# Optimization experiments

Measured on AMD Instinct MI355X. Metric: run time of the kernel, lower is better.

Reference implementation:

```python
import jax, jax.numpy as jnp
import numpy as np

N_LOC, D_IN = 100000, 128
N_ROUTES, ROUTE_LEN = 8192, 100
D_OUT = 256
LN_EPS = 1e-5


def setup_inputs() -> dict:
    key = jax.random.key(0)
    k1, k2, k3 = jax.random.split(key, 3)
    graph_embedding = jax.random.normal(k1, (N_LOC, D_IN), dtype=jnp.float32)
    locations_idx = jax.random.randint(k2, (N_ROUTES, ROUTE_LEN), 0, N_LOC, dtype=jnp.int64)
    W = jax.random.normal(k3, (D_IN, D_OUT), dtype=jnp.float32) / np.sqrt(D_IN)
    b = jnp.zeros((D_OUT,), dtype=jnp.float32)
    gamma = jnp.ones((D_OUT,), dtype=jnp.float32)
    beta = jnp.zeros((D_OUT,), dtype=jnp.float32)
    return {"graph_embedding": graph_embedding, "locations_idx": locations_idx,
            "W": W, "b": b, "gamma": gamma, "beta": beta}


def reference(graph_embedding, locations_idx, W, b, gamma, beta):
    # Gather per-route node embeddings: [n_routes, route_len, D_in]
    gathered = graph_embedding[locations_idx]
    # Max-pool over the route dimension -> [n_routes, D_in]
    pooled = jnp.max(gathered, axis=1)
    # LinearBlockWithNormalization: Linear -> LayerNorm -> ReLU
    h = pooled @ W + b  # [n_routes, D_out]
    mu = jnp.mean(h, axis=-1, keepdims=True)
    var = jnp.mean(jnp.square(h - mu), axis=-1, keepdims=True)
    hn = (h - mu) * jax.lax.rsqrt(var + LN_EPS) * gamma + beta
    return jax.nn.relu(hn)
```

## Files before the change

kernel.cpp:

```cpp
#include <hip/hip_runtime.h>
#include <math.h>

constexpr int N_LOC     = 100000;
constexpr int D_IN      = 128;
constexpr int N_ROUTES  = 8192;
constexpr int ROUTE_LEN = 100;
constexpr int D_OUT     = 256;
constexpr float LN_EPS  = 1e-5f;

constexpr int RPB      = 4;
constexpr int NTHREADS = 256;
constexpr size_t EMB_ELEMS = (size_t)N_LOC * D_IN;
constexpr size_t F16_BYTES = EMB_ELEMS * 2;

typedef __fp16 f16x2 __attribute__((ext_vector_type(2)));

__device__ inline unsigned pk_max_f16(unsigned a, unsigned b) {
    unsigned d;
    asm("v_pk_max_f16 %0, %1, %2" : "=v"(d) : "v"(a), "v"(b));
    return d;
}

__global__ __launch_bounds__(256, 8)
void convert_f16_kernel(const float* __restrict__ emb, unsigned* __restrict__ emb16) {
    size_t i = ((size_t)blockIdx.x * blockDim.x + threadIdx.x) * 4;
    const size_t stride = (size_t)gridDim.x * blockDim.x * 4;
    for (; i < EMB_ELEMS; i += stride) {
        const float4 v = *reinterpret_cast<const float4*>(emb + i);
        const f16x2 a = __builtin_amdgcn_cvt_pkrtz(v.x, v.y);
        const f16x2 b = __builtin_amdgcn_cvt_pkrtz(v.z, v.w);
        uint2 u;
        u.x = __builtin_bit_cast(unsigned, a);
        u.y = __builtin_bit_cast(unsigned, b);
        *reinterpret_cast<uint2*>(emb16 + i / 2) = u;
    }
}

template<bool F16>
__global__ __launch_bounds__(NTHREADS, 8)
void routes_encoder_kernel(const float*    __restrict__ emb,
                           const unsigned* __restrict__ emb16,
                           const int*      __restrict__ idx,
                           const float*    __restrict__ W,
                           const float*    __restrict__ bias,
                           const float*    __restrict__ gamma,
                           const float*    __restrict__ beta,
                           float*          __restrict__ out)
{
    __shared__ int   s_idx[RPB * ROUTE_LEN];
    __shared__ float s_pooled[RPB][D_IN];
    __shared__ float s_sum[4][RPB];
    __shared__ float s_ssq[4][RPB];

    const int tid    = threadIdx.x;
    const int route0 = blockIdx.x * RPB;

    for (int i = tid; i < RPB * ROUTE_LEN; i += NTHREADS)
        s_idx[i] = idx[(size_t)route0 * ROUTE_LEN + i];
    __syncthreads();

    const int w    = tid >> 6;
    const int lane = tid & 63;

    if constexpr (F16) {
        const int q  = lane >> 4;
        const int dc = (lane & 15) * 8;
        const int* gi = &s_idx[w * ROUTE_LEN];
        unsigned m0 = 0xFC00FC00u, m1 = m0, m2 = m0, m3 = m0;
        #pragma unroll 5
        for (int t = 0; t < ROUTE_LEN / 4; ++t) {
            const int row = gi[4 * t + q];
            const uint4 v = *reinterpret_cast<const uint4*>(
                emb16 + ((size_t)row * D_IN + dc) / 2);
            m0 = pk_max_f16(m0, v.x);
            m1 = pk_max_f16(m1, v.y);
            m2 = pk_max_f16(m2, v.z);
            m3 = pk_max_f16(m3, v.w);
        }
        #pragma unroll
        for (int off = 32; off >= 16; off >>= 1) {
            m0 = pk_max_f16(m0, (unsigned)__shfl_down((int)m0, off));
            m1 = pk_max_f16(m1, (unsigned)__shfl_down((int)m1, off));
            m2 = pk_max_f16(m2, (unsigned)__shfl_down((int)m2, off));
            m3 = pk_max_f16(m3, (unsigned)__shfl_down((int)m3, off));
        }
        if (lane < 16) {
            const f16x2 h0 = __builtin_bit_cast(f16x2, m0);
            const f16x2 h1 = __builtin_bit_cast(f16x2, m1);
            const f16x2 h2 = __builtin_bit_cast(f16x2, m2);
            const f16x2 h3 = __builtin_bit_cast(f16x2, m3);
            *reinterpret_cast<float4*>(&s_pooled[w][dc]) =
                make_float4((float)h0.x, (float)h0.y, (float)h1.x, (float)h1.y);
            *reinterpret_cast<float4*>(&s_pooled[w][dc + 4]) =
                make_float4((float)h2.x, (float)h2.y, (float)h3.x, (float)h3.y);
        }
    } else {
        const int* gi = &s_idx[w * ROUTE_LEN];
        float2 m = make_float2(-INFINITY, -INFINITY);
        #pragma unroll 10
        for (int l = 0; l < ROUTE_LEN; ++l) {
            const float2 v = *reinterpret_cast<const float2*>(
                emb + (size_t)gi[l] * D_IN + lane * 2);
            m.x = fmaxf(m.x, v.x);
            m.y = fmaxf(m.y, v.y);
        }
        *reinterpret_cast<float2*>(&s_pooled[w][lane * 2]) = m;
    }
    __syncthreads();

    float h[RPB];
    {
        const float bo = bias[tid];
        #pragma unroll
        for (int r = 0; r < RPB; ++r) h[r] = bo;

        #pragma unroll 8
        for (int k = 0; k < D_IN; k += 4) {
            const float wk0 = W[(size_t)(k + 0) * D_OUT + tid];
            const float wk1 = W[(size_t)(k + 1) * D_OUT + tid];
            const float wk2 = W[(size_t)(k + 2) * D_OUT + tid];
            const float wk3 = W[(size_t)(k + 3) * D_OUT + tid];
            #pragma unroll
            for (int r = 0; r < RPB; ++r) {
                const float4 p = *reinterpret_cast<const float4*>(&s_pooled[r][k]);
                h[r] = fmaf(p.x, wk0, h[r]);
                h[r] = fmaf(p.y, wk1, h[r]);
                h[r] = fmaf(p.z, wk2, h[r]);
                h[r] = fmaf(p.w, wk3, h[r]);
            }
        }
    }

    float s[RPB], ss[RPB];
    #pragma unroll
    for (int r = 0; r < RPB; ++r) { s[r] = h[r]; ss[r] = h[r] * h[r]; }

    #pragma unroll
    for (int off = 32; off > 0; off >>= 1) {
        #pragma unroll
        for (int r = 0; r < RPB; ++r) {
            s[r]  += __shfl_down(s[r],  off);
            ss[r] += __shfl_down(ss[r], off);
        }
    }
    if (lane == 0) {
        #pragma unroll
        for (int r = 0; r < RPB; ++r) { s_sum[w][r] = s[r]; s_ssq[w][r] = ss[r]; }
    }
    __syncthreads();

    const float gm = gamma[tid];
    const float bt = beta[tid];
    #pragma unroll
    for (int r = 0; r < RPB; ++r) {
        const float tot = s_sum[0][r] + s_sum[1][r] + s_sum[2][r] + s_sum[3][r];
        const float tsq = s_ssq[0][r] + s_ssq[1][r] + s_ssq[2][r] + s_ssq[3][r];
        const float mu  = tot * (1.0f / D_OUT);
        const float var = tsq * (1.0f / D_OUT) - mu * mu;
        const float inv = rsqrtf(var + LN_EPS);
        const float y   = fmaxf((h[r] - mu) * inv * gm + bt, 0.0f);
        __builtin_nontemporal_store(y, &out[(size_t)(route0 + r) * D_OUT + tid]);
    }
}

extern "C" void kernel_launch(void* const* d_in, const int* in_sizes, int n_in,
                              void* d_out, int out_size, void* d_ws, size_t ws_size,
                              hipStream_t stream) {
    const float* emb   = (const float*)d_in[0];
    const int*   idx   = (const int*)  d_in[1];
    const float* W     = (const float*)d_in[2];
    const float* bias  = (const float*)d_in[3];
    const float* gamma = (const float*)d_in[4];
    const float* beta  = (const float*)d_in[5];
    float* out = (float*)d_out;

    if (ws_size >= F16_BYTES) {
        unsigned* emb16 = (unsigned*)d_ws;
        convert_f16_kernel<<<dim3(2048), dim3(256), 0, stream>>>(emb, emb16);
        routes_encoder_kernel<true><<<dim3(N_ROUTES / RPB), dim3(NTHREADS), 0, stream>>>(
            emb, emb16, idx, W, bias, gamma, beta, out);
    } else {
        routes_encoder_kernel<false><<<dim3(N_ROUTES / RPB), dim3(NTHREADS), 0, stream>>>(
            emb, nullptr, idx, W, bias, gamma, beta, out);
    }
}
```

Before: 139.9 us.

## Split gather-max into row-range passes for cache locality, then reduce partials

The embedding table is split into 8 row ranges, and a new pass computes per-route partial maxima using only indices inside each range, selected via ballot masks. The idea is that each range's slice of the fp16 table stays resident in cache. A second pass combines the 8 partials and runs the linear, LayerNorm and ReLU epilogue. In exchange it launches 8x more blocks, scans indices redundantly, serializes the per-index loads within each wave, and writes and reads an extra partial buffer.

```diff
diff --git a/kernel.cpp b/kernel.cpp
--- a/kernel.cpp
+++ b/kernel.cpp
@@ -8,10 +8,14 @@
 constexpr int D_OUT     = 256;
 constexpr float LN_EPS  = 1e-5f;
 
+constexpr int NRANGE   = 8;
+constexpr int RSIZE    = N_LOC / NRANGE;
 constexpr int RPB      = 4;
 constexpr int NTHREADS = 256;
-constexpr size_t EMB_ELEMS = (size_t)N_LOC * D_IN;
-constexpr size_t F16_BYTES = EMB_ELEMS * 2;
+constexpr size_t EMB_ELEMS  = (size_t)N_LOC * D_IN;
+constexpr size_t F16_BYTES  = EMB_ELEMS * 2;
+constexpr size_t PART_U32S  = (size_t)NRANGE * N_ROUTES * (D_IN / 2);
+constexpr size_t PART_BYTES = PART_U32S * 4;
 
 typedef __fp16 f16x2 __attribute__((ext_vector_type(2)));
 
@@ -33,6 +37,134 @@
         u.x = __builtin_bit_cast(unsigned, a);
         u.y = __builtin_bit_cast(unsigned, b);
         *reinterpret_cast<uint2*>(emb16 + i / 2) = u;
+    }
+}
+
+__global__ __launch_bounds__(NTHREADS, 8)
+void pass_a_kernel(const unsigned* __restrict__ emb16,
+                   const int*      __restrict__ idx,
+                   unsigned*       __restrict__ part)
+{
+    __shared__ int s_idx[RPB * ROUTE_LEN];
+
+    const int tid    = threadIdx.x;
+    const int range  = blockIdx.x & (NRANGE - 1);
+    const int rgrp   = blockIdx.x >> 3;
+    const int route0 = rgrp * RPB;
+
+    for (int i = tid; i < RPB * ROUTE_LEN; i += NTHREADS)
+        s_idx[i] = idx[(size_t)route0 * ROUTE_LEN + i];
+    __syncthreads();
+
+    const int w    = tid >> 6;
+    const int lane = tid & 63;
+    const int* gi  = &s_idx[w * ROUTE_LEN];
+    const int  lo  = range * RSIZE;
+
+    const int i0 = gi[lane];
+    const int i1 = (lane < ROUTE_LEN - 64) ? gi[64 + lane] : -1;
+    unsigned long long m0 = __ballot((unsigned)(i0 - lo) < (unsigned)RSIZE);
+    unsigned long long m1 = __ballot(i1 >= 0 && (unsigned)(i1 - lo) < (unsigned)RSIZE);
+
+    unsigned acc0 = 0xFC00FC00u, acc1 = 0xFC00FC00u;
+    while (m0 | m1) {
+        if (m0) {
+            const int l = __ffsll((unsigned long long)m0) - 1; m0 &= m0 - 1;
+            const unsigned v = emb16[(size_t)gi[l] * (D_IN / 2) + lane];
+            acc0 = pk_max_f16(acc0, v);
+        }
+        if (m1) {
+            const int l = __ffsll((unsigned long long)m1) - 1; m1 &= m1 - 1;
+            const unsigned v = emb16[(size_t)gi[64 + l] * (D_IN / 2) + lane];
+            acc1 = pk_max_f16(acc1, v);
+        }
+    }
+    const unsigned acc = pk_max_f16(acc0, acc1);
+    __builtin_nontemporal_store(
+        acc, &part[((size_t)range * N_ROUTES + route0 + w) * (D_IN / 2) + lane]);
+}
+
+__global__ __launch_bounds__(NTHREADS, 8)
+void pass_b_kernel(const unsigned* __restrict__ part,
+                   const float*    __restrict__ W,
+                   const float*    __restrict__ bias,
+                   const float*    __restrict__ gamma,
+                   const float*    __restrict__ beta,
+                   float*          __restrict__ out)
+{
+    __shared__ float s_pooled[RPB][D_IN];
+    __shared__ float s_sum[4][RPB];
+    __shared__ float s_ssq[4][RPB];
+
+    const int tid    = threadIdx.x;
+    const int route0 = blockIdx.x * RPB;
+    const int w      = tid >> 6;
+    const int lane   = tid & 63;
+
+    {
+        const int route = route0 + w;
+        unsigned acc = 0xFC00FC00u;
+        #pragma unroll
+        for (int k = 0; k < NRANGE; ++k)
+            acc = pk_max_f16(acc, part[((size_t)k * N_ROUTES + route) * (D_IN / 2) + lane]);
+        const f16x2 h = __builtin_bit_cast(f16x2, acc);
+        s_pooled[w][2 * lane]     = (float)h.x;
+        s_pooled[w][2 * lane + 1] = (float)h.y;
+    }
+    __syncthreads();
+
+    float h[RPB];
+    {
+        const float bo = bias[tid];
+        #pragma unroll
+        for (int r = 0; r < RPB; ++r) h[r] = bo;
+
+        #pragma unroll 8
+        for (int k = 0; k < D_IN; k += 4) {
+            const float wk0 = W[(size_t)(k + 0) * D_OUT + tid];
+            const float wk1 = W[(size_t)(k + 1) * D_OUT + tid];
+            const float wk2 = W[(size_t)(k + 2) * D_OUT + tid];
+            const float wk3 = W[(size_t)(k + 3) * D_OUT + tid];
+            #pragma unroll
+            for (int r = 0; r < RPB; ++r) {
+                const float4 p = *reinterpret_cast<const float4*>(&s_pooled[r][k]);
+                h[r] = fmaf(p.x, wk0, h[r]);
+                h[r] = fmaf(p.y, wk1, h[r]);
+                h[r] = fmaf(p.z, wk2, h[r]);
+                h[r] = fmaf(p.w, wk3, h[r]);
+            }
+        }
+    }
+
+    float s[RPB], ss[RPB];
+    #pragma unroll
+    for (int r = 0; r < RPB; ++r) { s[r] = h[r]; ss[r] = h[r] * h[r]; }
+
+    #pragma unroll
+    for (int off = 32; off > 0; off >>= 1) {
+        #pragma unroll
+        for (int r = 0; r < RPB; ++r) {
+            s[r]  += __shfl_down(s[r],  off);
+            ss[r] += __shfl_down(ss[r], off);
+        }
+    }
+    if (lane == 0) {
+        #pragma unroll
+        for (int r = 0; r < RPB; ++r) { s_sum[w][r] = s[r]; s_ssq[w][r] = ss[r]; }
+    }
+    __syncthreads();
+
+    const float gm = gamma[tid];
+    const float bt = beta[tid];
+    #pragma unroll
+    for (int r = 0; r < RPB; ++r) {
+        const float tot = s_sum[0][r] + s_sum[1][r] + s_sum[2][r] + s_sum[3][r];
+        const float tsq = s_ssq[0][r] + s_ssq[1][r] + s_ssq[2][r] + s_ssq[3][r];
+        const float mu  = tot * (1.0f / D_OUT);
+        const float var = tsq * (1.0f / D_OUT) - mu * mu;
+        const float inv = rsqrtf(var + LN_EPS);
+        const float y   = fmaxf((h[r] - mu) * inv * gm + bt, 0.0f);
+        __builtin_nontemporal_store(y, &out[(size_t)(route0 + r) * D_OUT + tid]);
     }
 }
 
@@ -113,7 +245,6 @@
         const float bo = bias[tid];
         #pragma unroll
         for (int r = 0; r < RPB; ++r) h[r] = bo;
-
         #pragma unroll 8
         for (int k = 0; k < D_IN; k += 4) {
             const float wk0 = W[(size_t)(k + 0) * D_OUT + tid];
@@ -134,7 +265,6 @@
     float s[RPB], ss[RPB];
     #pragma unroll
     for (int r = 0; r < RPB; ++r) { s[r] = h[r]; ss[r] = h[r] * h[r]; }
-
     #pragma unroll
     for (int off = 32; off > 0; off >>= 1) {
         #pragma unroll
@@ -174,7 +304,15 @@
     const float* beta  = (const float*)d_in[5];
     float* out = (float*)d_out;
 
-    if (ws_size >= F16_BYTES) {
+    if (ws_size >= F16_BYTES + PART_BYTES) {
+        unsigned* emb16 = (unsigned*)d_ws;
+        unsigned* part  = (unsigned*)((char*)d_ws + F16_BYTES);
+        convert_f16_kernel<<<dim3(2048), dim3(256), 0, stream>>>(emb, emb16);
+        pass_a_kernel<<<dim3((N_ROUTES / RPB) * NRANGE), dim3(NTHREADS), 0, stream>>>(
+            emb16, idx, part);
+        pass_b_kernel<<<dim3(N_ROUTES / RPB), dim3(NTHREADS), 0, stream>>>(
+            part, W, bias, gamma, beta, out);
+    } else if (ws_size >= F16_BYTES) {
         unsigned* emb16 = (unsigned*)d_ws;
         convert_f16_kernel<<<dim3(2048), dim3(256), 0, stream>>>(emb, emb16);
         routes_encoder_kernel<true><<<dim3(N_ROUTES / RPB), dim3(NTHREADS), 0, stream>>>(
```

After: 163.8 us. +17.1%, slower.
